# Performance work log

Measured on AMD Instinct MI355X. Metric: run time of the kernel, lower is better.

Reference implementation:

```python
import jax, jax.numpy as jnp
import numpy as np

N_NODES = 50000
N_EDGES = 800000
D_FEAT = 128
HIDDEN = 128
OUT = 64
HEADS = 4


def setup_inputs() -> dict:
    key = jax.random.key(0)
    ks = jax.random.split(key, 12)
    s_in = 1.0 / np.sqrt(D_FEAT)
    s_h = 1.0 / np.sqrt(HIDDEN)
    x = jax.random.normal(ks[0], (N_NODES, D_FEAT), dtype=jnp.float32)
    edge_index = jax.random.randint(ks[1], (2, N_EDGES), 0, N_NODES, dtype=jnp.int32)
    return {
        "x": x,
        "edge_index": edge_index,
        # SAGEConv params: lin_l (aggregated neighbors), lin_r (root), bias
        "W_l": jax.random.normal(ks[2], (D_FEAT, HIDDEN), dtype=jnp.float32) * s_in,
        "W_r": jax.random.normal(ks[3], (D_FEAT, HIDDEN), dtype=jnp.float32) * s_in,
        "b_sage": jnp.zeros((HIDDEN,), dtype=jnp.float32),
        # GATConv params: lin_src, lin_dst (heads*hidden each), att vectors, bias
        "W_src": jax.random.normal(ks[4], (HIDDEN, HEADS * HIDDEN), dtype=jnp.float32) * s_h,
        "W_dst": jax.random.normal(ks[5], (HIDDEN, HEADS * HIDDEN), dtype=jnp.float32) * s_h,
        "att_src": jax.random.normal(ks[6], (HEADS, HIDDEN), dtype=jnp.float32) * s_h,
        "att_dst": jax.random.normal(ks[7], (HEADS, HIDDEN), dtype=jnp.float32) * s_h,
        "b_gat": jnp.zeros((HIDDEN,), dtype=jnp.float32),
        # Final Linear
        "W_lin": jax.random.normal(ks[8], (HIDDEN, OUT), dtype=jnp.float32) * s_h,
        "b_lin": jnp.zeros((OUT,), dtype=jnp.float32),
    }


def reference(x, edge_index, W_l, W_r, b_sage, W_src, W_dst, att_src, att_dst, b_gat, W_lin, b_lin):
    N = x.shape[0]
    src = edge_index[0]
    dst = edge_index[1]

    # ---- SAGEConv (mean aggregation): out = lin_l(mean_j x_j) + lin_r(x_i) + b ----
    agg = jax.ops.segment_sum(x[src], dst, num_segments=N)          # [N, d]
    cnt = jax.ops.segment_sum(jnp.ones_like(dst, dtype=x.dtype), dst, num_segments=N)
    mean_nbr = agg / jnp.maximum(cnt, 1.0)[:, None]
    h = mean_nbr @ W_l + x @ W_r + b_sage                           # [N, H*... no: [N, hidden]
    h = jax.nn.relu(h)

    # ---- GATConv (heads=4, concat=False -> mean over heads) ----
    H, C = att_src.shape
    hs = (h @ W_src).reshape(N, H, C)                               # source-transformed [N, H, C]
    hd = (h @ W_dst).reshape(N, H, C)                               # dest-transformed   [N, H, C]
    a_s = jnp.einsum('nhc,hc->nh', hs, att_src)                     # [N, H]
    a_d = jnp.einsum('nhc,hc->nh', hd, att_dst)                     # [N, H]
    e = jax.nn.leaky_relu(a_s[src] + a_d[dst], negative_slope=0.2)  # [E, H]
    # edge softmax over incoming edges per destination node
    e_max = jax.ops.segment_max(e, dst, num_segments=N)             # [N, H]
    e_exp = jnp.exp(e - e_max[dst])                                 # [E, H]
    denom = jax.ops.segment_sum(e_exp, dst, num_segments=N)         # [N, H]
    alpha = e_exp / denom[dst]                                      # [E, H]
    msg = hs[src] * alpha[:, :, None]                               # [E, H, C]
    out = jax.ops.segment_sum(msg, dst, num_segments=N)             # [N, H, C]
    out = out.mean(axis=1) + b_gat                                  # concat=False: avg heads
    out = jax.nn.relu(out)

    # ---- final Linear ----
    return out @ W_lin + b_lin
```

## Files before the change

### kernel.cpp

```cpp
#include <hip/hip_runtime.h>

#define D 128
#define HEADS 4

typedef __attribute__((ext_vector_type(8))) short short8;
typedef __attribute__((ext_vector_type(4))) float f32x4;
typedef __attribute__((ext_vector_type(2))) float f32x2;

static __device__ __forceinline__ float leaky(float v) { return v > 0.f ? v : 0.2f * v; }

static __device__ __forceinline__ f32x2 bf2_to_p2(unsigned int u) {
    union { unsigned int i; float f; } a, b;
    a.i = u << 16;
    b.i = u & 0xffff0000u;
    f32x2 r; r.x = a.f; r.y = b.f;
    return r;
}
static __device__ __forceinline__ float bf_to_f(unsigned short s) {
    union { unsigned int i; float f; } a;
    a.i = ((unsigned int)s) << 16;
    return a.f;
}
static __device__ __forceinline__ unsigned short f2bf(float f) {
    union { float f; unsigned int i; } v; v.f = f;
    unsigned int u = v.i;
    unsigned int r = (u + 0x7fffu + ((u >> 16) & 1u)) >> 16;
    return (unsigned short)r;
}

static __device__ __forceinline__ void pk_fma(f32x2& acc, f32x2 v, f32x2 w) {
    asm("v_pk_fma_f32 %0, %1, %2, %0" : "+v"(acc) : "v"(v), "v"(w));
}
static __device__ __forceinline__ void pk_fma_lo(f32x2& acc, f32x2 v, f32x2 w) {
    asm("v_pk_fma_f32 %0, %1, %2, %0 op_sel:[0,0,0] op_sel_hi:[1,0,1]"
        : "+v"(acc) : "v"(v), "v"(w));
}
static __device__ __forceinline__ void pk_fma_hi(f32x2& acc, f32x2 v, f32x2 w) {
    asm("v_pk_fma_f32 %0, %1, %2, %0 op_sel:[0,1,0] op_sel_hi:[1,1,1]"
        : "+v"(acc) : "v"(v), "v"(w));
}
static __device__ __forceinline__ void pk_add(f32x2& acc, f32x2 v) {
    asm("v_pk_add_f32 %0, %1, %0" : "+v"(acc) : "v"(v));
}

#define CPAD 16
#define PREP_CNT 107520
#define MAXBUCK 2048
#define BSLOT 1024
#define CH 8192

__global__ __launch_bounds__(256) void k_early(const float* __restrict__ x, int npairs,
                                               const int* __restrict__ ei, int E, int nbuck, int scatB,
                                               int* __restrict__ bcur,
                                               unsigned int* __restrict__ ebuf,
                                               const float* __restrict__ Wl, const float* __restrict__ Wr,
                                               const float* __restrict__ Wsrc, const float* __restrict__ Wlin,
                                               const float* __restrict__ Wdst,
                                               const float* __restrict__ atts, const float* __restrict__ attd,
                                               unsigned short* __restrict__ Bh,
                                               unsigned short* __restrict__ Bg,
                                               unsigned short* __restrict__ Bf,
                                               float* __restrict__ wsd,
                                               unsigned int* __restrict__ xb) {
    __shared__ unsigned int sval[CH];
    __shared__ unsigned short soff[CH];
    __shared__ int cnt[MAXBUCK];
    __shared__ int gbase[MAXBUCK];
    int gb = blockIdx.x, t = threadIdx.x;
    if (gb < scatB) {
        int c0 = gb * CH;
        int ecnt = E - c0; if (ecnt > CH) ecnt = CH;
        for (int i = t; i < MAXBUCK; i += 256) cnt[i] = 0;
        __syncthreads();
        for (int i = t; i < ecnt; i += 256) {
            int s = ei[c0 + i], d = ei[E + c0 + i];
            int b = d >> 5;
            soff[i] = (unsigned short)atomicAdd(&cnt[b], 1);
            sval[i] = (unsigned int)s | ((unsigned int)(d & 31) << 16) | ((unsigned int)b << 21);
        }
        __syncthreads();
        for (int b = t; b < nbuck; b += 256)
            if (cnt[b]) gbase[b] = (b << 10) + atomicAdd(&bcur[b * CPAD], cnt[b]);
        __syncthreads();
        for (int i = t; i < ecnt; i += 256) {
            unsigned int v = sval[i];
            int b = v >> 21;
            int pos = gbase[b] + soff[i];
            if (pos < ((b + 1) << 10)) ebuf[pos] = v & 0x1fffffu;
        }
        return;
    }
    int i = (gb - scatB) * 256 + t;
    if (i < 32768) {
        int idx = i;
        int j = idx & 7, n16 = (idx >> 3) & 15, quad = (idx >> 7) & 3, rest = idx >> 9;
        int nc = rest & 7, kb = rest >> 3;
        int kk = kb * 32 + quad * 8 + j;
        int n = nc * 16 + n16;
        float v = (kk < 128) ? Wl[kk * 128 + n] : Wr[(kk - 128) * 128 + n];
        Bh[idx] = f2bf(v);
    } else if (i < 32768 + 65536) {
        int idx = i - 32768;
        int j = idx & 7, n16 = (idx >> 3) & 15, quad = (idx >> 7) & 3, rest = idx >> 9;
        int nc = rest & 7, kb = rest >> 3;
        int kk = kb * 32 + quad * 8 + j;
        int n = nc * 16 + n16;
        float v = Wsrc[(kk & 127) * 512 + (kk >> 7) * 128 + n];
        Bg[idx] = f2bf(v);
    } else if (i < 32768 + 65536 + 8192) {
        int idx = i - 98304;
        int j = idx & 7, n16 = (idx >> 3) & 15, quad = (idx >> 7) & 3, rest = idx >> 9;
        int nc = rest & 3, kb = rest >> 2;
        int kk = kb * 32 + quad * 8 + j;
        int n = nc * 16 + n16;
        Bf[idx] = f2bf(Wlin[kk * 64 + n]);
    } else if (i < PREP_CNT) {
        int tt = i - 106496;
        int k = tt >> 3, o = tt & 7;
        int hh = o & 3;
        const float* W = (o < 4) ? Wsrc : Wdst;
        const float* att = (o < 4) ? atts : attd;
        float acc = 0.f;
        for (int c = 0; c < 128; c++) acc += W[k * 512 + hh * 128 + c] * att[hh * 128 + c];
        wsd[o * 132 + k] = acc;
    } else {
        int p = i - PREP_CNT;
        if (p < npairs) {
            float2 v = *(const float2*)(x + (size_t)p * 2);
            xb[p] = (unsigned int)f2bf(v.x) | ((unsigned int)f2bf(v.y) << 16);
        }
    }
}

#define BCAP 1024
__global__ __launch_bounds__(256) void k_build_sage(const unsigned int* __restrict__ ebuf,
                                                    const int* __restrict__ bcur,
                                                    const unsigned int* __restrict__ xb,
                                                    int* __restrict__ csr,
                                                    int* __restrict__ rowptr,
                                                    int* __restrict__ rowend,
                                                    unsigned int* __restrict__ meanb, int N) {
    __shared__ int cnt[32];
    __shared__ int excl[33];
    __shared__ unsigned char off[BCAP];
    __shared__ unsigned int rawv[BCAP];
    __shared__ int sorted[BCAP];
    int b = blockIdx.x, t = threadIdx.x;
    int e0 = b << 10;
    int ecnt = bcur[b * CPAD];
    if (ecnt > BCAP) ecnt = BCAP;
    if (t < 32) cnt[t] = 0;
    __syncthreads();
    for (int i = t; i < ecnt; i += 256) {
        unsigned int p = ebuf[e0 + i];
        rawv[i] = p;
        off[i] = (unsigned char)atomicAdd(&cnt[(p >> 16) & 31], 1);
    }
    __syncthreads();
    if (t == 0) {
        int run = 0;
        #pragma unroll
        for (int j = 0; j < 32; j++) { excl[j] = run; run += cnt[j]; }
        excl[32] = run;
    }
    __syncthreads();
    for (int i = t; i < ecnt; i += 256) {
        unsigned int p = rawv[i];
        int d = (p >> 16) & 31;
        sorted[excl[d] + off[i]] = (int)((p & 0xffffu) << 6);
    }
    __syncthreads();
    int nb0 = b << 5;
    if (t < 32 && nb0 + t < N) {
        rowptr[nb0 + t] = e0 + excl[t];
        rowend[nb0 + t] = e0 + excl[t + 1];
    }
    for (int i = t; i < ecnt; i += 256) csr[e0 + i] = sorted[i];
    int wv = t >> 6, lane = t & 63;
    for (int k = 0; k < 8; k++) {
        int local = wv * 8 + k;
        int node = nb0 + local;
        if (node >= N) continue;
        int le0 = excl[local], le1 = excl[local + 1];
        f32x2 aA = {0.f, 0.f}, aB = {0.f, 0.f};
        int e = le0;
        for (; e + 3 < le1; e += 4) {
            int s0 = sorted[e], s1 = sorted[e + 1], s2 = sorted[e + 2], s3 = sorted[e + 3];
            unsigned int u0 = xb[(unsigned)(s0 + lane)];
            unsigned int u1 = xb[(unsigned)(s1 + lane)];
            unsigned int u2 = xb[(unsigned)(s2 + lane)];
            unsigned int u3 = xb[(unsigned)(s3 + lane)];
            pk_add(aA, bf2_to_p2(u0));
            pk_add(aB, bf2_to_p2(u1));
            pk_add(aA, bf2_to_p2(u2));
            pk_add(aB, bf2_to_p2(u3));
        }
        for (; e < le1; e++)
            pk_add(aA, bf2_to_p2(xb[(unsigned)(sorted[e] + lane)]));
        pk_add(aA, aB);
        int dg = le1 - le0;
        float inv = 1.0f / (float)(dg > 0 ? dg : 1);
        unsigned int o = (unsigned int)f2bf(aA.x * inv) | ((unsigned int)f2bf(aA.y * inv) << 16);
        __builtin_nontemporal_store(o, meanb + (size_t)node * 64 + lane);
    }
}

__global__ __launch_bounds__(256) void k_mfma_h(const unsigned short* __restrict__ A0,
                                                const unsigned short* __restrict__ A1,
                                                const unsigned short* __restrict__ Bp,
                                                const float* __restrict__ bias,
                                                const float* __restrict__ wsd,
                                                unsigned short* __restrict__ outb,
                                                float* __restrict__ a_s,
                                                float* __restrict__ a_d, int M) {
    const int NC = 8;
    __shared__ unsigned short sH[64][136];
    __shared__ float swsd[1056];
    int tid = threadIdx.x;
    int wave = tid >> 6;
    int lane = tid & 63;
    int row0 = blockIdx.x * 64 + wave * 16;
    int n16 = lane & 15, quad = lane >> 4;
    int arow = row0 + n16;
    int arowc = arow < M ? arow : 0;
    for (int i = tid; i < 1056; i += 256) swsd[i] = wsd[i];
    f32x4 acc[NC];
    #pragma unroll
    for (int i = 0; i < NC; i++) acc[i] = (f32x4){0.f, 0.f, 0.f, 0.f};
    #pragma unroll
    for (int kb = 0; kb < 8; kb++) {
        const unsigned short* ap = (kb < 4)
            ? (A0 + (size_t)arowc * 128 + kb * 32 + quad * 8)
            : (A1 + (size_t)arowc * 128 + (kb - 4) * 32 + quad * 8);
        short8 af = *(const short8*)ap;
        #pragma unroll
        for (int nc = 0; nc < NC; nc++) {
            short8 bf = *(const short8*)(Bp + ((((size_t)(kb * NC + nc) * 4 + quad) * 16 + n16) << 3));
            acc[nc] = __builtin_amdgcn_mfma_f32_16x16x32_bf16(af, bf, acc[nc], 0, 0, 0);
        }
    }
    int orow = row0 + quad * 4;
    int lrow = wave * 16 + quad * 4;
    #pragma unroll
    for (int r = 0; r < 4; r++) {
        int m = orow + r;
        #pragma unroll
        for (int nc = 0; nc < NC; nc++) {
            int col = nc * 16 + n16;
            float v = fmaxf(acc[nc][r] + bias[col], 0.f);
            unsigned short bv = f2bf(v);
            sH[lrow + r][col] = bv;
            if (m < M) outb[(size_t)m * 128 + col] = bv;
        }
    }
    __syncthreads();
    #pragma unroll
    for (int j = tid; j < 512; j += 256) {
        int m = j >> 3, o = j & 7;
        const float* wr = swsd + o * 132;
        f32x2 pa = {0.f, 0.f}, pb = {0.f, 0.f};
        #pragma unroll 4
        for (int kb = 0; kb < 16; kb++) {
            const unsigned int* hp = (const unsigned int*)&sH[m][kb * 8];
            unsigned int h0 = hp[0], h1 = hp[1], h2 = hp[2], h3 = hp[3];
            f32x4 wa = *(const f32x4*)(wr + kb * 8);
            f32x4 wb = *(const f32x4*)(wr + kb * 8 + 4);
            pk_fma(pa, bf2_to_p2(h0), __builtin_shufflevector(wa, wa, 0, 1));
            pk_fma(pb, bf2_to_p2(h1), __builtin_shufflevector(wa, wa, 2, 3));
            pk_fma(pa, bf2_to_p2(h2), __builtin_shufflevector(wb, wb, 0, 1));
            pk_fma(pb, bf2_to_p2(h3), __builtin_shufflevector(wb, wb, 2, 3));
        }
        pk_add(pa, pb);
        float accd = pa.x + pa.y;
        int n = blockIdx.x * 64 + m;
        if (n < M) {
            if (o < 4) a_s[n * 4 + o] = accd;
            else       a_d[n * 4 + (o - 4)] = accd;
        }
    }
}

#define EDGE_CAP 192
__global__ __launch_bounds__(256) void k_gat_agg(const int* __restrict__ rowptr,
                                                 const int* __restrict__ rowend,
                                                 const int* __restrict__ csr,
                                                 const unsigned int* __restrict__ hb,
                                                 const float* __restrict__ a_s,
                                                 const float* __restrict__ a_d,
                                                 unsigned int* __restrict__ aggb, int N) {
    __shared__ int   sSrc[4][EDGE_CAP];
    __shared__ float sAl[4][EDGE_CAP * 4];
    int wv = threadIdx.x >> 6;
    int lane = threadIdx.x & 63;
    int n = blockIdx.x * 4 + wv;
    bool active = n < N;
    int e0 = 0, deg = 0;
    float4 ad = {0.f, 0.f, 0.f, 0.f};
    if (active) {
        e0 = rowptr[n];
        deg = rowend[n] - e0;
        ad = *(const float4*)(a_d + (size_t)n * 4);
    }
    f32x4 psum = {0.f, 0.f, 0.f, 0.f};
    for (int base = 0; base < deg; base += 64) {
        int i = base + lane;
        if (i < deg) {
            int s64 = csr[e0 + i];
            float4 as = *(const float4*)(a_s + (size_t)(s64 >> 4));
            f32x4 w;
            w.x = __expf(leaky(as.x + ad.x));
            w.y = __expf(leaky(as.y + ad.y));
            w.z = __expf(leaky(as.z + ad.z));
            w.w = __expf(leaky(as.w + ad.w));
            psum += w;
            if (i < EDGE_CAP) {
                sSrc[wv][i] = s64;
                *(f32x4*)&sAl[wv][i * 4] = w;
            }
        }
    }
    #pragma unroll
    for (int o = 32; o; o >>= 1) {
        psum.x += __shfl_xor(psum.x, o);
        psum.y += __shfl_xor(psum.y, o);
        psum.z += __shfl_xor(psum.z, o);
        psum.w += __shfl_xor(psum.w, o);
    }
    f32x4 inv;
    inv.x = psum.x > 0.f ? 0.25f / psum.x : 0.f;
    inv.y = psum.y > 0.f ? 0.25f / psum.y : 0.f;
    inv.z = psum.z > 0.f ? 0.25f / psum.z : 0.f;
    inv.w = psum.w > 0.f ? 0.25f / psum.w : 0.f;
    int capdeg = deg < EDGE_CAP ? deg : EDGE_CAP;
    for (int base = 0; base < capdeg; base += 64) {
        int i = base + lane;
        if (i < capdeg) {
            f32x4 w = *(f32x4*)&sAl[wv][i * 4];
            w *= inv;
            *(f32x4*)&sAl[wv][i * 4] = w;
        }
    }
    __syncthreads();
    f32x2 ac0 = {0.f, 0.f}, ac1 = {0.f, 0.f}, ac2 = {0.f, 0.f}, ac3 = {0.f, 0.f};
    int e = 0;
    for (; e + 3 < capdeg; e += 4) {
        int o0 = sSrc[wv][e], o1 = sSrc[wv][e + 1], o2 = sSrc[wv][e + 2], o3 = sSrc[wv][e + 3];
        f32x4 w0 = *(const f32x4*)&sAl[wv][e * 4];
        f32x4 w1 = *(const f32x4*)&sAl[wv][e * 4 + 4];
        f32x4 w2 = *(const f32x4*)&sAl[wv][e * 4 + 8];
        f32x4 w3 = *(const f32x4*)&sAl[wv][e * 4 + 12];
        unsigned int u0 = hb[(unsigned)(o0 + lane)];
        unsigned int u1 = hb[(unsigned)(o1 + lane)];
        unsigned int u2 = hb[(unsigned)(o2 + lane)];
        unsigned int u3 = hb[(unsigned)(o3 + lane)];
        f32x2 v0 = bf2_to_p2(u0), v1 = bf2_to_p2(u1), v2 = bf2_to_p2(u2), v3 = bf2_to_p2(u3);
        f32x2 w0a = __builtin_shufflevector(w0, w0, 0, 1), w0b = __builtin_shufflevector(w0, w0, 2, 3);
        f32x2 w1a = __builtin_shufflevector(w1, w1, 0, 1), w1b = __builtin_shufflevector(w1, w1, 2, 3);
        f32x2 w2a = __builtin_shufflevector(w2, w2, 0, 1), w2b = __builtin_shufflevector(w2, w2, 2, 3);
        f32x2 w3a = __builtin_shufflevector(w3, w3, 0, 1), w3b = __builtin_shufflevector(w3, w3, 2, 3);
        pk_fma_lo(ac0, v0, w0a); pk_fma_hi(ac1, v0, w0a); pk_fma_lo(ac2, v0, w0b); pk_fma_hi(ac3, v0, w0b);
        pk_fma_lo(ac0, v1, w1a); pk_fma_hi(ac1, v1, w1a); pk_fma_lo(ac2, v1, w1b); pk_fma_hi(ac3, v1, w1b);
        pk_fma_lo(ac0, v2, w2a); pk_fma_hi(ac1, v2, w2a); pk_fma_lo(ac2, v2, w2b); pk_fma_hi(ac3, v2, w2b);
        pk_fma_lo(ac0, v3, w3a); pk_fma_hi(ac1, v3, w3a); pk_fma_lo(ac2, v3, w3b); pk_fma_hi(ac3, v3, w3b);
    }
    for (; e < capdeg; e++) {
        int o0 = sSrc[wv][e];
        f32x4 w0 = *(const f32x4*)&sAl[wv][e * 4];
        f32x2 v0 = bf2_to_p2(hb[(unsigned)(o0 + lane)]);
        f32x2 wa = __builtin_shufflevector(w0, w0, 0, 1), wb = __builtin_shufflevector(w0, w0, 2, 3);
        pk_fma_lo(ac0, v0, wa); pk_fma_hi(ac1, v0, wa);
        pk_fma_lo(ac2, v0, wb); pk_fma_hi(ac3, v0, wb);
    }
    for (int i = EDGE_CAP; i < deg; i++) {
        int s64 = csr[e0 + i];
        float4 as = *(const float4*)(a_s + (size_t)(s64 >> 4));
        f32x4 w;
        w.x = __expf(leaky(as.x + ad.x)) * inv.x;
        w.y = __expf(leaky(as.y + ad.y)) * inv.y;
        w.z = __expf(leaky(as.z + ad.z)) * inv.z;
        w.w = __expf(leaky(as.w + ad.w)) * inv.w;
        f32x2 v0 = bf2_to_p2(hb[(unsigned)(s64 + lane)]);
        f32x2 wa = __builtin_shufflevector(w, w, 0, 1), wb = __builtin_shufflevector(w, w, 2, 3);
        pk_fma_lo(ac0, v0, wa); pk_fma_hi(ac1, v0, wa);
        pk_fma_lo(ac2, v0, wb); pk_fma_hi(ac3, v0, wb);
    }
    if (!active) return;
    unsigned int* rowu = aggb + (size_t)n * 256 + lane;
    unsigned int o0 = (unsigned int)f2bf(ac0.x) | ((unsigned int)f2bf(ac0.y) << 16);
    unsigned int o1 = (unsigned int)f2bf(ac1.x) | ((unsigned int)f2bf(ac1.y) << 16);
    unsigned int o2 = (unsigned int)f2bf(ac2.x) | ((unsigned int)f2bf(ac2.y) << 16);
    unsigned int o3 = (unsigned int)f2bf(ac3.x) | ((unsigned int)f2bf(ac3.y) << 16);
    __builtin_nontemporal_store(o0, rowu + 0);
    __builtin_nontemporal_store(o1, rowu + 64);
    __builtin_nontemporal_store(o2, rowu + 128);
    __builtin_nontemporal_store(o3, rowu + 192);
}

__global__ __launch_bounds__(256) void k_mfma_tail(const unsigned short* __restrict__ aggb,
                                                   const unsigned short* __restrict__ Bg,
                                                   const float* __restrict__ bg,
                                                   const unsigned short* __restrict__ Bf,
                                                   const float* __restrict__ bl,
                                                   float* __restrict__ out, int M) {
    __shared__ unsigned short sG[64][136];
    int wave = threadIdx.x >> 6;
    int lane = threadIdx.x & 63;
    int row0 = blockIdx.x * 64 + wave * 16;
    int n16 = lane & 15, quad = lane >> 4;
    {
        int arow = row0 + n16;
        int arowc = arow < M ? arow : 0;
        const unsigned short* ap = aggb + (size_t)arowc * 512 + quad * 8;
        f32x4 acc[8];
        #pragma unroll
        for (int i = 0; i < 8; i++) acc[i] = (f32x4){0.f, 0.f, 0.f, 0.f};
        #pragma unroll
        for (int kb = 0; kb < 16; kb++) {
            short8 af = *(const short8*)(ap + kb * 32);
            #pragma unroll
            for (int nc = 0; nc < 8; nc++) {
                short8 bf = *(const short8*)(Bg + ((((size_t)(kb * 8 + nc) * 4 + quad) * 16 + n16) << 3));
                acc[nc] = __builtin_amdgcn_mfma_f32_16x16x32_bf16(af, bf, acc[nc], 0, 0, 0);
            }
        }
        int lrow = wave * 16 + quad * 4;
        #pragma unroll
        for (int r = 0; r < 4; r++) {
            #pragma unroll
            for (int nc = 0; nc < 8; nc++) {
                int col = nc * 16 + n16;
                sG[lrow + r][col] = f2bf(fmaxf(acc[nc][r] + bg[col], 0.f));
            }
        }
    }
    __syncthreads();
    {
        f32x4 acc[4];
        #pragma unroll
        for (int i = 0; i < 4; i++) acc[i] = (f32x4){0.f, 0.f, 0.f, 0.f};
        #pragma unroll
        for (int kb = 0; kb < 4; kb++) {
            short8 af = *(const short8*)&sG[wave * 16 + n16][kb * 32 + quad * 8];
            #pragma unroll
            for (int nc = 0; nc < 4; nc++) {
                short8 bf = *(const short8*)(Bf + ((((size_t)(kb * 4 + nc) * 4 + quad) * 16 + n16) << 3));
                acc[nc] = __builtin_amdgcn_mfma_f32_16x16x32_bf16(af, bf, acc[nc], 0, 0, 0);
            }
        }
        int orow = row0 + quad * 4;
        #pragma unroll
        for (int r = 0; r < 4; r++) {
            int m = orow + r;
            if (m < M) {
                #pragma unroll
                for (int nc = 0; nc < 4; nc++) {
                    int col = nc * 16 + n16;
                    out[(size_t)m * 64 + col] = acc[nc][r] + bl[col];
                }
            }
        }
    }
}

extern "C" void kernel_launch(void* const* d_in, const int* in_sizes, int n_in,
                              void* d_out, int out_size, void* d_ws, size_t ws_size,
                              hipStream_t stream) {
    const float* x    = (const float*)d_in[0];
    const int*   ei   = (const int*)d_in[1];
    const float* Wl   = (const float*)d_in[2];
    const float* Wr   = (const float*)d_in[3];
    const float* bs   = (const float*)d_in[4];
    const float* Wsrc = (const float*)d_in[5];
    const float* Wdst = (const float*)d_in[6];
    const float* atts = (const float*)d_in[7];
    const float* attd = (const float*)d_in[8];
    const float* bg   = (const float*)d_in[9];
    const float* Wlin = (const float*)d_in[10];
    const float* bl   = (const float*)d_in[11];
    int N = in_sizes[0] / D;
    int E = in_sizes[1] / 2;
    int nbuck = (N + 31) >> 5;
    int npairs = N * 64;

    char* w = (char*)d_ws;
    auto alloc = [&](size_t bytes) {
        char* p = w;
        w += (bytes + 255) & ~(size_t)255;
        return p;
    };
    unsigned int* xb     = (unsigned int*)alloc((size_t)N * 256);
    unsigned int* meanb  = (unsigned int*)alloc((size_t)N * 256);
    unsigned int* hb     = (unsigned int*)alloc((size_t)N * 256);
    unsigned int* aggb   = (unsigned int*)alloc((size_t)N * 1024);
    unsigned short* Bh   = (unsigned short*)alloc(65536 * 2);
    unsigned short* Bg   = (unsigned short*)alloc(65536 * 2);
    unsigned short* Bf   = (unsigned short*)alloc(8192 * 2);
    float* a_s           = (float*)alloc((size_t)N * 16);
    float* a_d           = (float*)alloc((size_t)N * 16);
    float* wsd           = (float*)alloc(1056 * 4);
    int* rowptr          = (int*)alloc((size_t)N * 4);
    int* rowend          = (int*)alloc((size_t)N * 4);
    int* bcur            = (int*)alloc((size_t)MAXBUCK * CPAD * 4);
    unsigned int* ebuf   = (unsigned int*)alloc((size_t)MAXBUCK * BSLOT * 4);
    int* csr             = (int*)alloc((size_t)MAXBUCK * BSLOT * 4);
    (void)ws_size; (void)n_in; (void)out_size;

    hipMemsetAsync(bcur, 0, (size_t)MAXBUCK * CPAD * 4, stream);

    int scatB = (E + CH - 1) / CH;
    int workBlocks = (PREP_CNT + npairs + 255) / 256;
    k_early<<<scatB + workBlocks, 256, 0, stream>>>(x, npairs, ei, E, nbuck, scatB,
                                                    bcur, ebuf,
                                                    Wl, Wr, Wsrc, Wlin, Wdst, atts, attd,
                                                    Bh, Bg, Bf, wsd, xb);
    k_build_sage<<<nbuck, 256, 0, stream>>>(ebuf, bcur, xb, csr, rowptr, rowend, meanb, N);

    k_mfma_h<<<(N + 63) / 64, 256, 0, stream>>>((const unsigned short*)meanb,
                                                (const unsigned short*)xb, Bh, bs, wsd,
                                                (unsigned short*)hb, a_s, a_d, N);
    k_gat_agg<<<(N + 3) / 4, 256, 0, stream>>>(rowptr, rowend, csr, hb, a_s, a_d, aggb, N);
    k_mfma_tail<<<(N + 63) / 64, 256, 0, stream>>>((const unsigned short*)aggb, Bg, bg,
                                                   Bf, bl, (float*)d_out, N);
}
```

Measured before the change: 240.4 us.

## Use hardware bf16 pack, shrink GAT blocks, drop barrier, split LDS loads

```diff
diff --git a/kernel.cpp b/kernel.cpp
--- a/kernel.cpp
+++ b/kernel.cpp
@@ -16,16 +16,16 @@
     f32x2 r; r.x = a.f; r.y = b.f;
     return r;
 }
-static __device__ __forceinline__ float bf_to_f(unsigned short s) {
-    union { unsigned int i; float f; } a;
-    a.i = ((unsigned int)s) << 16;
-    return a.f;
-}
 static __device__ __forceinline__ unsigned short f2bf(float f) {
     union { float f; unsigned int i; } v; v.f = f;
     unsigned int u = v.i;
     unsigned int r = (u + 0x7fffu + ((u >> 16) & 1u)) >> 16;
     return (unsigned short)r;
+}
+static __device__ __forceinline__ unsigned int packbf(f32x2 v) {
+    unsigned int r;
+    asm("v_cvt_pk_bf16_f32 %0, %1, %2" : "=v"(r) : "v"(v.x), "v"(v.y));
+    return r;
 }
 
 static __device__ __forceinline__ void pk_fma(f32x2& acc, f32x2 v, f32x2 w) {
@@ -127,7 +127,7 @@
         int p = i - PREP_CNT;
         if (p < npairs) {
             float2 v = *(const float2*)(x + (size_t)p * 2);
-            xb[p] = (unsigned int)f2bf(v.x) | ((unsigned int)f2bf(v.y) << 16);
+            xb[p] = packbf((f32x2){v.x, v.y});
         }
     }
 }
@@ -200,7 +200,8 @@
         pk_add(aA, aB);
         int dg = le1 - le0;
         float inv = 1.0f / (float)(dg > 0 ? dg : 1);
-        unsigned int o = (unsigned int)f2bf(aA.x * inv) | ((unsigned int)f2bf(aA.y * inv) << 16);
+        f32x2 sm = aA; sm.x *= inv; sm.y *= inv;
+        unsigned int o = packbf(sm);
         __builtin_nontemporal_store(o, meanb + (size_t)node * 64 + lane);
     }
 }
@@ -263,12 +264,14 @@
         for (int kb = 0; kb < 16; kb++) {
             const unsigned int* hp = (const unsigned int*)&sH[m][kb * 8];
             unsigned int h0 = hp[0], h1 = hp[1], h2 = hp[2], h3 = hp[3];
-            f32x4 wa = *(const f32x4*)(wr + kb * 8);
-            f32x4 wb = *(const f32x4*)(wr + kb * 8 + 4);
-            pk_fma(pa, bf2_to_p2(h0), __builtin_shufflevector(wa, wa, 0, 1));
-            pk_fma(pb, bf2_to_p2(h1), __builtin_shufflevector(wa, wa, 2, 3));
-            pk_fma(pa, bf2_to_p2(h2), __builtin_shufflevector(wb, wb, 0, 1));
-            pk_fma(pb, bf2_to_p2(h3), __builtin_shufflevector(wb, wb, 2, 3));
+            f32x2 wa0 = *(const f32x2*)(wr + kb * 8);
+            f32x2 wa1 = *(const f32x2*)(wr + kb * 8 + 2);
+            f32x2 wb0 = *(const f32x2*)(wr + kb * 8 + 4);
+            f32x2 wb1 = *(const f32x2*)(wr + kb * 8 + 6);
+            pk_fma(pa, bf2_to_p2(h0), wa0);
+            pk_fma(pb, bf2_to_p2(h1), wa1);
+            pk_fma(pa, bf2_to_p2(h2), wb0);
+            pk_fma(pb, bf2_to_p2(h3), wb1);
         }
         pk_add(pa, pb);
         float accd = pa.x + pa.y;
@@ -281,18 +284,18 @@
 }
 
 #define EDGE_CAP 192
-__global__ __launch_bounds__(256) void k_gat_agg(const int* __restrict__ rowptr,
+__global__ __launch_bounds__(128) void k_gat_agg(const int* __restrict__ rowptr,
                                                  const int* __restrict__ rowend,
                                                  const int* __restrict__ csr,
                                                  const unsigned int* __restrict__ hb,
                                                  const float* __restrict__ a_s,
                                                  const float* __restrict__ a_d,
                                                  unsigned int* __restrict__ aggb, int N) {
-    __shared__ int   sSrc[4][EDGE_CAP];
-    __shared__ float sAl[4][EDGE_CAP * 4];
+    __shared__ int   sSrc[2][EDGE_CAP];
+    __shared__ float sAl[2][EDGE_CAP * 4];
     int wv = threadIdx.x >> 6;
     int lane = threadIdx.x & 63;
-    int n = blockIdx.x * 4 + wv;
+    int n = blockIdx.x * 2 + wv;
     bool active = n < N;
     int e0 = 0, deg = 0;
     float4 ad = {0.f, 0.f, 0.f, 0.f};
@@ -340,24 +343,23 @@
             *(f32x4*)&sAl[wv][i * 4] = w;
         }
     }
-    __syncthreads();
     f32x2 ac0 = {0.f, 0.f}, ac1 = {0.f, 0.f}, ac2 = {0.f, 0.f}, ac3 = {0.f, 0.f};
     int e = 0;
     for (; e + 3 < capdeg; e += 4) {
         int o0 = sSrc[wv][e], o1 = sSrc[wv][e + 1], o2 = sSrc[wv][e + 2], o3 = sSrc[wv][e + 3];
-        f32x4 w0 = *(const f32x4*)&sAl[wv][e * 4];
-        f32x4 w1 = *(const f32x4*)&sAl[wv][e * 4 + 4];
-        f32x4 w2 = *(const f32x4*)&sAl[wv][e * 4 + 8];
-        f32x4 w3 = *(const f32x4*)&sAl[wv][e * 4 + 12];
         unsigned int u0 = hb[(unsigned)(o0 + lane)];
         unsigned int u1 = hb[(unsigned)(o1 + lane)];
         unsigned int u2 = hb[(unsigned)(o2 + lane)];
         unsigned int u3 = hb[(unsigned)(o3 + lane)];
+        f32x2 w0a = *(const f32x2*)&sAl[wv][e * 4];
+        f32x2 w0b = *(const f32x2*)&sAl[wv][e * 4 + 2];
+        f32x2 w1a = *(const f32x2*)&sAl[wv][e * 4 + 4];
+        f32x2 w1b = *(const f32x2*)&sAl[wv][e * 4 + 6];
+        f32x2 w2a = *(const f32x2*)&sAl[wv][e * 4 + 8];
+        f32x2 w2b = *(const f32x2*)&sAl[wv][e * 4 + 10];
+        f32x2 w3a = *(const f32x2*)&sAl[wv][e * 4 + 12];
+        f32x2 w3b = *(const f32x2*)&sAl[wv][e * 4 + 14];
         f32x2 v0 = bf2_to_p2(u0), v1 = bf2_to_p2(u1), v2 = bf2_to_p2(u2), v3 = bf2_to_p2(u3);
-        f32x2 w0a = __builtin_shufflevector(w0, w0, 0, 1), w0b = __builtin_shufflevector(w0, w0, 2, 3);
-        f32x2 w1a = __builtin_shufflevector(w1, w1, 0, 1), w1b = __builtin_shufflevector(w1, w1, 2, 3);
-        f32x2 w2a = __builtin_shufflevector(w2, w2, 0, 1), w2b = __builtin_shufflevector(w2, w2, 2, 3);
-        f32x2 w3a = __builtin_shufflevector(w3, w3, 0, 1), w3b = __builtin_shufflevector(w3, w3, 2, 3);
         pk_fma_lo(ac0, v0, w0a); pk_fma_hi(ac1, v0, w0a); pk_fma_lo(ac2, v0, w0b); pk_fma_hi(ac3, v0, w0b);
         pk_fma_lo(ac0, v1, w1a); pk_fma_hi(ac1, v1, w1a); pk_fma_lo(ac2, v1, w1b); pk_fma_hi(ac3, v1, w1b);
         pk_fma_lo(ac0, v2, w2a); pk_fma_hi(ac1, v2, w2a); pk_fma_lo(ac2, v2, w2b); pk_fma_hi(ac3, v2, w2b);
@@ -365,9 +367,10 @@
     }
     for (; e < capdeg; e++) {
         int o0 = sSrc[wv][e];
-        f32x4 w0 = *(const f32x4*)&sAl[wv][e * 4];
-        f32x2 v0 = bf2_to_p2(hb[(unsigned)(o0 + lane)]);
-        f32x2 wa = __builtin_shufflevector(w0, w0, 0, 1), wb = __builtin_shufflevector(w0, w0, 2, 3);
+        unsigned int u0 = hb[(unsigned)(o0 + lane)];
+        f32x2 wa = *(const f32x2*)&sAl[wv][e * 4];
+        f32x2 wb = *(const f32x2*)&sAl[wv][e * 4 + 2];
+        f32x2 v0 = bf2_to_p2(u0);
         pk_fma_lo(ac0, v0, wa); pk_fma_hi(ac1, v0, wa);
         pk_fma_lo(ac2, v0, wb); pk_fma_hi(ac3, v0, wb);
     }
@@ -380,20 +383,16 @@
         w.z = __expf(leaky(as.z + ad.z)) * inv.z;
         w.w = __expf(leaky(as.w + ad.w)) * inv.w;
         f32x2 v0 = bf2_to_p2(hb[(unsigned)(s64 + lane)]);
-        f32x2 wa = __builtin_shufflevector(w, w, 0, 1), wb = __builtin_shufflevector(w, w, 2, 3);
+        f32x2 wa = {w.x, w.y}, wb = {w.z, w.w};
         pk_fma_lo(ac0, v0, wa); pk_fma_hi(ac1, v0, wa);
         pk_fma_lo(ac2, v0, wb); pk_fma_hi(ac3, v0, wb);
     }
     if (!active) return;
     unsigned int* rowu = aggb + (size_t)n * 256 + lane;
-    unsigned int o0 = (unsigned int)f2bf(ac0.x) | ((unsigned int)f2bf(ac0.y) << 16);
-    unsigned int o1 = (unsigned int)f2bf(ac1.x) | ((unsigned int)f2bf(ac1.y) << 16);
-    unsigned int o2 = (unsigned int)f2bf(ac2.x) | ((unsigned int)f2bf(ac2.y) << 16);
-    unsigned int o3 = (unsigned int)f2bf(ac3.x) | ((unsigned int)f2bf(ac3.y) << 16);
-    __builtin_nontemporal_store(o0, rowu + 0);
-    __builtin_nontemporal_store(o1, rowu + 64);
-    __builtin_nontemporal_store(o2, rowu + 128);
-    __builtin_nontemporal_store(o3, rowu + 192);
+    __builtin_nontemporal_store(packbf(ac0), rowu + 0);
+    __builtin_nontemporal_store(packbf(ac1), rowu + 64);
+    __builtin_nontemporal_store(packbf(ac2), rowu + 128);
+    __builtin_nontemporal_store(packbf(ac3), rowu + 192);
 }
 
 __global__ __launch_bounds__(256) void k_mfma_tail(const unsigned short* __restrict__ aggb,
@@ -518,7 +517,7 @@
     k_mfma_h<<<(N + 63) / 64, 256, 0, stream>>>((const unsigned short*)meanb,
                                                 (const unsigned short*)xb, Bh, bs, wsd,
                                                 (unsigned short*)hb, a_s, a_d, N);
-    k_gat_agg<<<(N + 3) / 4, 256, 0, stream>>>(rowptr, rowend, csr, hb, a_s, a_d, aggb, N);
+    k_gat_agg<<<(N + 1) / 2, 128, 0, stream>>>(rowptr, rowend, csr, hb, a_s, a_d, aggb, N);
     k_mfma_tail<<<(N + 63) / 64, 256, 0, stream>>>((const unsigned short*)aggb, Bg, bg,
                                                    Bf, bl, (float*)d_out, N);
 }
```

Result: no change. 240.3 us (-0.1%).
